# Optimization experiments

Measured on AMD Instinct MI355X. Metric: run time of the kernel, lower is better.

The kernel has to match this reference:

```python
import jax, jax.numpy as jnp
import numpy as np

E, B, T = 7, 50, 100               # ensemble (network_size), no_batches=50, time blocks
D, A, L, H, C = 128, 32, 256, 1024, 128  # data, action, latent, hidden, context sizes
H_STEP = 0.1                        # (t1 - t0) / T == dt -> one SDE step per block


def setup_inputs() -> dict:
    key = jax.random.key(0)
    ks = iter(jax.random.split(key, 64))
    def nrm(shape, scale=1.0):
        return jax.random.normal(next(ks), shape, jnp.float32) * scale
    def ens(i, o):
        s = 1.0 / np.sqrt(i)
        return nrm((E, i, o), s), nrm((E, o), s)
    def lin(i, o):
        s = 1.0 / np.sqrt(i)
        return nrm((i, o), s), nrm((o,), s)
    inp = {}
    inp["enc_w1"], inp["enc_b1"] = ens(D, H)
    inp["enc_w2"], inp["enc_b2"] = ens(H, H)
    inp["enc_w3"], inp["enc_b3"] = ens(H, C)
    inp["qz0_w"], inp["qz0_b"] = ens(C, 2 * L)
    inp["act_w"], inp["act_b"] = ens(L + A + D, L)
    inp["proj_w1"], inp["proj_b1"] = ens(L, H)
    inp["proj_w2"], inp["proj_b2"] = ens(H, H)
    inp["proj_w3"], inp["proj_b3"] = ens(H, D)
    inp["f_w1"], inp["f_b1"] = lin(L, H)
    inp["f_w2"], inp["f_b2"] = lin(H, H)
    inp["f_w3"], inp["f_b3"] = lin(H, L)
    inp["h_w1"], inp["h_b1"] = lin(L, H)
    inp["h_w2"], inp["h_b2"] = lin(H, H)
    inp["h_w3"], inp["h_b3"] = lin(H, L)
    # per-latent-dim g nets: Linear(1,H) -> ReLU -> Linear(H,1), stacked over L dims
    inp["g_w1"] = nrm((L, H), 0.2)
    inp["g_b1"] = nrm((L, H), 0.2)
    inp["g_w2"] = nrm((L, H), 0.2 / np.sqrt(H))
    inp["g_b2"] = 0.5 + nrm((L,), 0.01)   # keep diffusion bounded away from 0
    inp["pz0_mean"] = jnp.zeros((E, 1, L), jnp.float32)
    inp["pz0_logstd"] = jnp.zeros((E, 1, L), jnp.float32)
    inp["xs"] = nrm((E, T * B, D))
    inp["actions"] = nrm((E, T * B, A))
    inp["eps_z0"] = nrm((T, E, B, L))      # torch.randn_like noise for z0 reparam
    inp["dw_noise"] = nrm((T, E * B, L))   # Brownian increment noise (unit std)
    return inp


def reference(enc_w1, enc_b1, enc_w2, enc_b2, enc_w3, enc_b3,
              qz0_w, qz0_b, act_w, act_b,
              proj_w1, proj_b1, proj_w2, proj_b2, proj_w3, proj_b3,
              f_w1, f_b1, f_w2, f_b2, f_w3, f_b3,
              h_w1, h_b1, h_w2, h_b2, h_w3, h_b3,
              g_w1, g_b1, g_w2, g_b2,
              pz0_mean, pz0_logstd,
              xs, actions, eps_z0, dw_noise):
    def ens_lin(x, w, b):  # EnsembleFC: bmm + bias
        return jnp.einsum('ebi,eio->ebo', x, w) + b[:, None, :]

    def encoder(x):
        x = jax.nn.relu(ens_lin(x, enc_w1, enc_b1))
        x = jax.nn.relu(ens_lin(x, enc_w2, enc_b2))
        return ens_lin(x, enc_w3, enc_b3)

    def projector(z):
        z = jnp.tanh(ens_lin(z, proj_w1, proj_b1))
        z = jnp.tanh(ens_lin(z, proj_w2, proj_b2))
        return ens_lin(z, proj_w3, proj_b3)

    def mlp(y, w1, b1, w2, b2, w3, b3):  # Linear-ReLU-Linear-Tanh-Linear
        y = jax.nn.relu(y @ w1 + b1)
        y = jnp.tanh(y @ w2 + b2)
        return y @ w3 + b3

    def g_fn(y):  # vectorized per-dim tiny MLPs: y (N, L) -> (N, L)
        hh = jax.nn.relu(y[:, :, None] * g_w1[None] + g_b1[None])  # (N, L, H)
        return jnp.sum(hh * g_w2[None], axis=-1) + g_b2

    xs_t = jnp.moveaxis(xs.reshape(E, T, B, D), 1, 0)        # (T, E, B, D)
    act_t = jnp.moveaxis(actions.reshape(E, T, B, A), 1, 0)  # (T, E, B, A)
    sqrt_h = jnp.sqrt(jnp.float32(H_STEP))

    def step(carry, inps):
        zs_last, i = carry
        x_i, a_i, eps_i, dw_i = inps
        ctx = encoder(x_i)                                  # (E, B, C)
        q = ens_lin(ctx, qz0_w, qz0_b)                      # (E, B, 2L)
        qm, ql = q[..., :L], q[..., L:]
        z0 = qm + jnp.exp(ql) * eps_i
        z_in = jnp.where(i == 0, z0, zs_last)               # first step uses z0
        lad = jnp.concatenate([z_in, a_i, x_i], axis=2)
        z = ens_lin(lad, act_w, act_b).reshape(E * B, L)
        # one SDE step with logqp (f: posterior drift, h: prior drift, g: diffusion)
        fv = mlp(z, f_w1, f_b1, f_w2, f_b2, f_w3, f_b3)
        hv = mlp(z, h_w1, h_b1, h_w2, h_b2, h_w3, h_b3)
        gv = g_fn(z)
        u = (fv - hv) / gv
        lr = 0.5 * jnp.sum(u * u, axis=-1) * H_STEP         # (E*B,) log-ratio increment
        z_new = z + fv * H_STEP + gv * (sqrt_h * dw_i)
        zs_new = z_new.reshape(E, B, L)
        xm = projector(zs_new)                              # (E, B, D)
        # KL(q(z0) || p(z0)) for diagonal Gaussians
        kl = (pz0_logstd - ql) \
             + (jnp.exp(2.0 * ql) + (qm - pz0_mean) ** 2) / (2.0 * jnp.exp(2.0 * pz0_logstd)) \
             - 0.5
        logqp0 = kl.sum(axis=2).mean(axis=1)                # (E,)
        lr_mean = lr.reshape(E, B).mean(axis=1)             # (E,)
        return (zs_new, i + 1), (lr_mean, logqp0, xm)

    init = (jnp.zeros((E, B, L), xs.dtype), jnp.int32(0))
    (_, _), (lrm, lq0, xms) = jax.lax.scan(step, init, (xs_t, act_t, eps_z0, dw_noise))
    logqp_path = lrm.sum(axis=0) + lq0.sum(axis=0)          # (E,)
    predicted_xs = jnp.moveaxis(xms, 0, 1).reshape(E, T * B, D)
    return logqp_path, predicted_xs
```

## Files before the change

kernel.cpp:

```cpp
#include <hip/hip_runtime.h>
#include <hip/hip_bf16.h>
#include <math.h>

#define E_ 7
#define B_ 50
#define T_ 100
#define D_ 128
#define A_ 32
#define L_ 256
#define H_ 1024
#define C_ 128
#define EB_ 350
#define TB_ 5000
#define SQRTH 0.31622776601683794f

typedef __attribute__((ext_vector_type(8))) short s8v;
typedef __attribute__((ext_vector_type(4))) float f32x4;
typedef _Float16 f16x2 __attribute__((ext_vector_type(2)));
typedef __hip_bfloat16 bf16;

#define MFMA __builtin_amdgcn_mfma_f32_16x16x32_bf16

__device__ __forceinline__ int lswz(int row, int ck) {
  return (((ck & ~7) | ((ck ^ row) & 7)) << 3);
}
__device__ __forceinline__ int swzE(int r, int col) {
  const int ck = col >> 3;
  return (((ck & ~7) | ((ck ^ r) & 7)) << 3) + (col & 7);
}

struct BG {
  const bf16* A[8];
  const bf16* W[8];
  const float* bias[8];
  float* Cf[8];
  bf16* Cb[8];
};

template<int BM, int ACT, int OUT>
__global__ __launch_bounds__(256)
void bgemm(BG g, int M, int K, int lda, int ldw, int ldc) {
  __shared__ short As[BM * 64];
  __shared__ short Ws[128 * 64];
  const short* Ap = (const short*)g.A[blockIdx.z];
  const short* Wp = (const short*)g.W[blockIdx.z];
  const int bm = blockIdx.x * BM, bn = blockIdx.y * 128;
  const int tid = threadIdx.x;
  const int wv = tid >> 6, lane = tid & 63;
  const int wm0 = (wv >> 1) * (BM / 2), wn0 = (wv & 1) * 64;
  const int l15 = lane & 15, l4 = lane >> 4;
  constexpr int FM = BM / 32;
// ... 50 lines not shown
  float* Cf = g.Cf[blockIdx.z];
  bf16* Cb = g.Cb[blockIdx.z];
#pragma unroll
  for (int n = 0; n < 4; ++n) {
    const int col = bn + wn0 + n * 16 + l15;
    const float bv = bias ? bias[col] : 0.f;
#pragma unroll
    for (int m = 0; m < FM; ++m) {
#pragma unroll
      for (int j = 0; j < 4; ++j) {
        const int row = bm + wm0 + m * 16 + l4 * 4 + j;
        if (row < M) {
          float v = acc[m][n][j] + bv;
          if (ACT == 1) v = fmaxf(v, 0.f);
          if (ACT == 2) v = tanhf(v);
          if (OUT == 0) Cf[(size_t)row * ldc + col] = v;
          if (OUT == 1) Cb[(size_t)row * ldc + col] = __float2bfloat16(v);
        }
      }
    }
  }
}

__global__ __launch_bounds__(256)
void cvtT_kernel(const float* __restrict__ src, bf16* __restrict__ dst,
                 int K, int N, long ss, long ds) {
  __shared__ float t[32][33];
  src += (size_t)blockIdx.z * ss;
  dst += (size_t)blockIdx.z * ds;
  const int n0 = blockIdx.x * 32, k0 = blockIdx.y * 32;
  const int tx = threadIdx.x & 31, ty = threadIdx.x >> 5;
#pragma unroll
  for (int i = 0; i < 4; ++i)
    t[ty + 8 * i][tx] = src[(size_t)(k0 + ty + 8 * i) * N + n0 + tx];
  __syncthreads();
#pragma unroll
  for (int i = 0; i < 4; ++i)
    dst[(size_t)(n0 + ty + 8 * i) * K + k0 + tx] = __float2bfloat16(t[tx][ty + 8 * i]);
}

struct B4 { bf16 a, b, c, d; };
__global__ __launch_bounds__(256)
void cvt_kernel(const float* __restrict__ s, bf16* __restrict__ d, int n4) {
  const int i = blockIdx.x * 256 + threadIdx.x;
  if (i < n4) {
    const float4 v = ((const float4*)s)[i];
    B4 o = {__float2bfloat16(v.x), __float2bfloat16(v.y),
            __float2bfloat16(v.z), __float2bfloat16(v.w)};
    ((B4*)d)[i] = o;
  }
}

__global__ __launch_bounds__(256)
void packW(const float* __restrict__ src, bf16* __restrict__ dst, int K, int N) {
  const int idx = blockIdx.x * 256 + threadIdx.x;
  if (idx >= K * N) return;
  const int k = idx / N, n = idx - k * N;
  const size_t fo = ((size_t)(n >> 4) * (K >> 5) + (k >> 5)) * 512 +
                    (((k >> 3) & 3) << 7) + ((n & 15) << 3) + (k & 7);
  dst[fo] = __float2bfloat16(src[idx]);
}

__global__ __launch_bounds__(256)
void packWz(const float* __restrict__ act_w, bf16* __restrict__ hi, bf16* __restrict__ lo) {
  const int idx = blockIdx.x * 256 + threadIdx.x;
  if (idx >= E_ * 65536) return;
  const int e = idx >> 16, rem = idx & 65535, k = rem >> 8, n = rem & 255;
  const float w = act_w[(size_t)e * 416 * 256 + (size_t)k * 256 + n];
  const bf16 h = __float2bfloat16(w);
  const size_t fo = (size_t)e * 65536 + ((size_t)(n >> 4) * 8 + (k >> 5)) * 512 +
                    (((k >> 3) & 3) << 7) + ((n & 15) << 3) + (k & 7);
  hi[fo] = h;
  lo[fo] = __float2bfloat16(w - __bfloat162float(h));
}

__global__ __launch_bounds__(256)
void ax_build(const float* __restrict__ actions, const float* __restrict__ xs,
              bf16* __restrict__ dst) {
  const int idx = blockIdx.x * 256 + threadIdx.x;
  if (idx >= E_ * TB_ * 192) return;
  const int k = idx % 192;
  const int r = (idx / 192) % TB_;
  const int e = idx / (192 * TB_);
// ... 4 lines not shown
}

__global__ __launch_bounds__(256)
void waxT_build(const float* __restrict__ act_w, bf16* __restrict__ dst) {
  const int idx = blockIdx.x * 256 + threadIdx.x;
  if (idx >= E_ * 256 * 192) return;
  const int k = idx % 192;
  const int n = (idx / 192) % 256;
  const int e = idx / (192 * 256);
  float v = (k < 160) ? act_w[(size_t)e * 416 * 256 + (size_t)(256 + k) * 256 + n] : 0.f;
  dst[idx] = __float2bfloat16(v);
}

__global__ __launch_bounds__(256)
void gpack_build(const float* __restrict__ gw1, const float* __restrict__ gb1,
                 const float* __restrict__ gw2, _Float16* __restrict__ dst) {
  const int idx = blockIdx.x * 256 + threadIdx.x;
  if (idx >= 256 * 3 * 1024) return;
  const int l = idx / 3072, rem = idx - l * 3072, arr = rem >> 10, h = rem & 1023;
  const float* s = arr == 0 ? gw1 : (arr == 1 ? gb1 : gw2);
  dst[idx] = (_Float16)s[(size_t)l * 1024 + h];
}

__global__ __launch_bounds__(256)
void qkl_kernel(const float* __restrict__ ctx, int rows, int row_off, int ctx_estride,
                const float* __restrict__ qw, const float* __restrict__ qb,
                const float* __restrict__ pm, const float* __restrict__ pl,
                const float* __restrict__ eps0, bf16* __restrict__ z0hi,
                bf16* __restrict__ z0lo, float* __restrict__ logqp) {
  __shared__ float cx[16][128];
  __shared__ float red[16];
  const int e = blockIdx.y;
  const int r0 = blockIdx.x * 16;
  const int tid = threadIdx.x;
  {
    const int r = tid >> 4, c = (tid & 15) * 8;
    float4 v0 = make_float4(0.f, 0.f, 0.f, 0.f), v1 = v0;
    if (r0 + r < rows) {
      const float* src = ctx + (size_t)e * ctx_estride + (size_t)(r0 + r) * C_ + c;
      v0 = *(const float4*)src;
      v1 = *(const float4*)(src + 4);
    }
    *(float4*)&cx[r][c] = v0;
    *(float4*)&cx[r][c + 4] = v1;
  }
  if (tid < 16) red[tid] = 0.f;
  __syncthreads();
  const int j = tid;
  const float* w = qw + (size_t)e * C_ * 512;
  float am_[16] = {};
  float al_[16] = {};
  for (int k0 = 0; k0 < C_; k0 += 4) {
    float wm[4], wl[4];
#pragma unroll
    for (int q = 0; q < 4; ++q) {
      wm[q] = w[(size_t)(k0 + q) * 512 + j];
      wl[q] = w[(size_t)(k0 + q) * 512 + 256 + j];
// ... 18 lines not shown
  for (int r = 0; r < 16; ++r) {
    float kl = 0.f;
    if (r0 + r < rows) {
      const float qm_ = am_[r] + qbm;
      const float ql_ = al_[r] + qbl;
      const float dm = qm_ - pmv;
      kl = plv - ql_ + (expf(2.f * ql_) + dm * dm) * inv2e - 0.5f;
      const int gi = row_off + r0 + r;
      if (gi < B_) {
        const size_t zi = ((size_t)e * B_ + gi) * L_ + j;
        const float z0 = qm_ + expf(ql_) * eps0[zi];
        const bf16 h = __float2bfloat16(z0);
        z0hi[zi] = h;
        z0lo[zi] = __float2bfloat16(z0 - __bfloat162float(h));
      }
    }
    for (int off = 32; off; off >>= 1) kl += __shfl_xor(kl, off, 64);
    if ((tid & 63) == 0) atomicAdd(&red[r], kl);
  }
  __syncthreads();
  if (tid < 16 && r0 + tid < rows) atomicAdd(&logqp[e], red[tid] * (1.0f / B_));
}

__global__ __launch_bounds__(256, 2)
void k1_act(const bf16* __restrict__ zhi, const bf16* __restrict__ zlo,
            const bf16* __restrict__ wzh, const bf16* __restrict__ wzl,
            const float* __restrict__ axw, float* __restrict__ zP,
            bf16* __restrict__ zPb, int t) {
  __shared__ short Ah[16 * 256];
  __shared__ short Al[16 * 256];
  const int e = blockIdx.z, rb = blockIdx.x, nb = blockIdx.y * 128;
  const int r0 = rb * 13;
  const int nrows = (50 - r0 < 13) ? (50 - r0) : 13;
  const int tid = threadIdx.x, lane = tid & 63, wv = tid >> 6;
  const int l15 = lane & 15, l4 = lane >> 4;
  const short* zh = (const short*)zhi + (size_t)(e * 50 + r0) * 256;
  const short* zl = (const short*)zlo + (size_t)(e * 50 + r0) * 256;
#pragma unroll
  for (int i = 0; i < 2; ++i) {
    const int lin = tid + i * 256, row = lin >> 5, ck = lin & 31;
    s8v vh = {}, vl = {};
    if (row < nrows) {
      vh = *(const s8v*)(zh + row * 256 + ck * 8);
      vl = *(const s8v*)(zl + row * 256 + ck * 8);
    }
    *(s8v*)(Ah + row * 256 + lswz(row, ck)) = vh;
    *(s8v*)(Al + row * 256 + lswz(row, ck)) = vl;
  }
  __syncthreads();
  const short* Bh = (const short*)wzh + (size_t)e * 65536;
  const short* Bl = (const short*)wzl + (size_t)e * 65536;
  f32x4 acc[2] = {};
#pragma unroll
  for (int kt = 0; kt < 8; ++kt) {
    const int ck = kt * 4 + l4;
    const s8v ah = *(const s8v*)(Ah + l15 * 256 + lswz(l15, ck));
    const s8v al = *(const s8v*)(Al + l15 * 256 + lswz(l15, ck));
// ... 7 lines not shown
      acc[nt] = MFMA(al, bh, acc[nt], 0, 0, 0);
      acc[nt] = MFMA(ah, bl, acc[nt], 0, 0, 0);
    }
  }
#pragma unroll
  for (int nt = 0; nt < 2; ++nt) {
    const int col = nb + wv * 32 + nt * 16 + l15;
#pragma unroll
    for (int j = 0; j < 4; ++j) {
      const int row = l4 * 4 + j;
      if (row < nrows) {
        const int gr = e * 50 + r0 + row;
        const float v = acc[nt][j] + axw[((size_t)e * TB_ + t * 50 + r0 + row) * 256 + col];
        zP[(size_t)gr * 256 + col] = v;
        zPb[(size_t)gr * 256 + col] = __float2bfloat16(v);
      }
    }
  }
}

__global__ __launch_bounds__(256, 2)
void k2_l1(const bf16* __restrict__ zPb, const bf16* __restrict__ w1f,
           const float* __restrict__ fb1, const float* __restrict__ hb1,
           bf16* __restrict__ fh1) {
  __shared__ short As[16 * 256];
  const int rb = blockIdx.x, nb = blockIdx.y * 128;
  const int r0 = rb * 16;
  const int tid = threadIdx.x, lane = tid & 63, wv = tid >> 6;
  const int l15 = lane & 15, l4 = lane >> 4;
#pragma unroll
  for (int i = 0; i < 2; ++i) {
    const int lin = tid + i * 256, row = lin >> 5, ck = lin & 31;
    s8v v = {};
    if (r0 + row < EB_)
      v = *(const s8v*)((const short*)zPb + (size_t)(r0 + row) * 256 + ck * 8);
    *(s8v*)(As + row * 256 + lswz(row, ck)) = v;
  }
  __syncthreads();
  f32x4 acc[2] = {};
#pragma unroll
  for (int kt = 0; kt < 8; ++kt) {
    const int ck = kt * 4 + l4;
    const s8v a = *(const s8v*)(As + l15 * 256 + lswz(l15, ck));
#pragma unroll
    for (int nt = 0; nt < 2; ++nt) {
      const int ng = nb + wv * 32 + nt * 16;
      const s8v b = *(const s8v*)((const short*)w1f + ((size_t)(ng >> 4) * 8 + kt) * 512 + lane * 8);
      acc[nt] = MFMA(a, b, acc[nt], 0, 0, 0);
    }
  }
#pragma unroll
  for (int nt = 0; nt < 2; ++nt) {
    const int col = nb + wv * 32 + nt * 16 + l15;
    const float bv = (col < 1024) ? fb1[col] : hb1[col - 1024];
#pragma unroll
    for (int j = 0; j < 4; ++j) {
      const int row = r0 + l4 * 4 + j;
      if (row < EB_)
        fh1[(size_t)row * 2048 + col] = __float2bfloat16(fmaxf(acc[nt][j] + bv, 0.f));
    }
  }
}

__global__ __launch_bounds__(256, 2)
void k3g(const bf16* __restrict__ fh1, const bf16* __restrict__ w2f,
         const float* __restrict__ fb2, const float* __restrict__ hb2,
         bf16* __restrict__ fh2, const float* __restrict__ zP,
         const _Float16* __restrict__ gpk, const float* __restrict__ gb2,
         float* __restrict__ gv) {
  __shared__ short As[16 * 1024];
  const int rb = blockIdx.x, nbl = blockIdx.y;
  const int tid = threadIdx.x, lane = tid & 63, wv = tid >> 6;
  const int l15 = lane & 15, l4 = lane >> 4;
  const int r0 = rb * 16;
  if (nbl >= 16) {
    float* ztile = (float*)As;
    const int c0 = (nbl - 16) * 64;
#pragma unroll
    for (int i = 0; i < 4; ++i) {
      const int lin = tid + i * 256, row = lin >> 6, col = lin & 63;
      ztile[row * 64 + col] =
          (r0 + row < EB_) ? zP[(size_t)(r0 + row) * 256 + c0 + col] : 1.0f;
    }
    __syncthreads();
    const int lloc = tid >> 2, hq = tid & 3;
    const _Float16* gl = gpk + (size_t)(c0 + lloc) * 3072 + hq * 256;
    f16x2 z2[16];
#pragma unroll
    for (int r = 0; r < 16; ++r) {
      const _Float16 zh_ = (_Float16)ztile[r * 64 + lloc];
      z2[r] = f16x2{zh_, zh_};
    }
    float ga[16] = {};
    for (int hp = 0; hp < 128; ++hp) {
      const f16x2 w1v = *(const f16x2*)(gl + 2 * hp);
      const f16x2 b1v = *(const f16x2*)(gl + 1024 + 2 * hp);
      const f16x2 w2v = *(const f16x2*)(gl + 2048 + 2 * hp);
// ... 46 lines not shown
      const s8v b = *(const s8v*)((const short*)w2f + ((size_t)(ng >> 4) * 32 + kt) * 512 + lane * 8);
      acc[nt] = MFMA(a, b, acc[nt], 0, 0, 0);
    }
  }
#pragma unroll
  for (int nt = 0; nt < 2; ++nt) {
    const int col = nb + wv * 32 + nt * 16 + l15;
    const float bv = half ? hb2[col - 1024] : fb2[col];
#pragma unroll
    for (int j = 0; j < 4; ++j) {
      const int row = r0 + l4 * 4 + j;
      if (row < EB_)
        fh2[(size_t)row * 2048 + col] = __float2bfloat16(tanhf(acc[nt][j] + bv));
    }
  }
}

__global__ __launch_bounds__(256, 1)
void k4_fin(const bf16* __restrict__ fh2, const bf16* __restrict__ w3f,
            const float* __restrict__ fb3, const float* __restrict__ hb3,
            const float* __restrict__ gv, const float* __restrict__ zP,
            const float* __restrict__ dw, bf16* __restrict__ zhi,
            bf16* __restrict__ zlo, bf16* __restrict__ zs_bf,
            float* __restrict__ logqp, int t) {
  __shared__ short As[16 * 1024];
  __shared__ float ztile[16][64];
  __shared__ float ebuck[8];
  const int rb = blockIdx.x, cb = blockIdx.y;
  const int r0 = rb * 16, c0 = cb * 64;
  const int tid = threadIdx.x, lane = tid & 63, wv = tid >> 6;
  const int l15 = lane & 15, l4 = lane >> 4;
  if (tid < 8) ebuck[tid] = 0.f;
#pragma unroll
  for (int i = 0; i < 4; ++i) {
    const int lin = tid + i * 256, row = lin >> 6, col = lin & 63;
    ztile[row][col] = (r0 + row < EB_) ? zP[(size_t)(r0 + row) * 256 + c0 + col] : 1.0f;
  }
  f32x4 accF = {}, accH = {};
#pragma unroll
  for (int fb = 0; fb < 2; ++fb) {
    __syncthreads();
#pragma unroll
    for (int i = 0; i < 8; ++i) {
      const int lin = tid + i * 256, row = lin >> 7, ck = lin & 127;
      s8v v = {};
      if (r0 + row < EB_)
        v = *(const s8v*)((const short*)fh2 + (size_t)(r0 + row) * 2048 + fb * 1024 + ck * 8);
      *(s8v*)(As + row * 1024 + lswz(row, ck)) = v;
    }
    __syncthreads();
    const int ng = fb * 256 + c0 + wv * 16;
    f32x4 acc = {};
#pragma unroll 4
    for (int kt = 0; kt < 32; ++kt) {
// ... 20 lines not shown
                         gvv * (SQRTH * dw[(size_t)t * (EB_ * 256) + (size_t)row * 256 + col]);
      const bf16 h = __float2bfloat16(znew);
      const size_t zi = (size_t)row * 256 + col;
      zhi[zi] = h;
      zlo[zi] = __float2bfloat16(znew - __bfloat162float(h));
      const int e = row / 50, b = row - e * 50;
      zs_bf[((size_t)e * TB_ + t * 50 + b) * 256 + col] = h;
    }
  }
  __syncthreads();
  if (tid < 7) {
    const float v = ebuck[tid];
    if (v != 0.f) atomicAdd(&logqp[tid], v);
  }
}

__global__ void init_kernel(float* logqp) {
  if (threadIdx.x < E_) logqp[threadIdx.x] = 0.f;
}

extern "C" void kernel_launch(void* const* d_in, const int* in_sizes, int n_in,
                              void* d_out, int out_size, void* d_ws, size_t ws_size,
                              hipStream_t stream) {
  (void)in_sizes; (void)n_in; (void)out_size;
  const float* enc_w1 = (const float*)d_in[0];
  const float* enc_b1 = (const float*)d_in[1];
  const float* enc_w2 = (const float*)d_in[2];
  const float* enc_b2 = (const float*)d_in[3];
  const float* enc_w3 = (const float*)d_in[4];
  const float* enc_b3 = (const float*)d_in[5];
  const float* qz0_w  = (const float*)d_in[6];
  const float* qz0_b  = (const float*)d_in[7];
  const float* act_w  = (const float*)d_in[8];
  const float* act_b  = (const float*)d_in[9];
  const float* proj_w1 = (const float*)d_in[10];
  const float* proj_b1 = (const float*)d_in[11];
  const float* proj_w2 = (const float*)d_in[12];
  const float* proj_b2 = (const float*)d_in[13];
  const float* proj_w3 = (const float*)d_in[14];
  const float* proj_b3 = (const float*)d_in[15];
  const float* f_w1 = (const float*)d_in[16];
  const float* f_b1 = (const float*)d_in[17];
  const float* f_w2 = (const float*)d_in[18];
  const float* f_b2 = (const float*)d_in[19];
  const float* f_w3 = (const float*)d_in[20];
  const float* f_b3 = (const float*)d_in[21];
  const float* h_w1 = (const float*)d_in[22];
// ... 22 lines not shown
  auto alloc = [&](size_t bytes) {
    void* p = base + off;
    off = (off + bytes + 255) & ~(size_t)255;
    return p;
  };
  bf16* zhi    = (bf16*)alloc((size_t)EB_ * 256 * 2);
  bf16* zlo    = (bf16*)alloc((size_t)EB_ * 256 * 2);
  float* zP    = (float*)alloc((size_t)EB_ * 256 * 4);
  bf16* zPb    = (bf16*)alloc((size_t)EB_ * 256 * 2);
  bf16* fh1    = (bf16*)alloc((size_t)EB_ * 2048 * 2);
  bf16* fh2    = (bf16*)alloc((size_t)EB_ * 2048 * 2);
  float* gvb   = (float*)alloc((size_t)EB_ * 256 * 4);
  bf16* zs_bf  = (bf16*)alloc((size_t)E_ * T_ * B_ * 256 * 2);
  float* axw   = (float*)alloc((size_t)E_ * TB_ * 256 * 4);
  bf16* ax_bf  = (bf16*)alloc((size_t)E_ * TB_ * 192 * 2);
  bf16* waxT   = (bf16*)alloc((size_t)E_ * 256 * 192 * 2);
  bf16* wzh    = (bf16*)alloc((size_t)E_ * 65536 * 2);
  bf16* wzl    = (bf16*)alloc((size_t)E_ * 65536 * 2);
  bf16* w1f    = (bf16*)alloc((size_t)2048 * 256 * 2);
  bf16* w2f    = (bf16*)alloc((size_t)2048 * 1024 * 2);
  bf16* w3f    = (bf16*)alloc((size_t)512 * 1024 * 2);
  _Float16* gpk = (_Float16*)alloc((size_t)256 * 3 * 1024 * 2);
  bf16* xs_bf  = (bf16*)alloc((size_t)E_ * TB_ * D_ * 2);
  bf16* ew1T = (bf16*)alloc((size_t)E_ * D_ * H_ * 2);
  bf16* ew2T = (bf16*)alloc((size_t)E_ * H_ * H_ * 2);
  bf16* ew3T = (bf16*)alloc((size_t)E_ * H_ * C_ * 2);
  bf16* pw1T = (bf16*)alloc((size_t)E_ * L_ * H_ * 2);
  bf16* pw2T = (bf16*)alloc((size_t)E_ * H_ * H_ * 2);
  bf16* pw3T = (bf16*)alloc((size_t)E_ * H_ * D_ * 2);
  const size_t per_row = (size_t)E_ * (H_ * 2 * 2 + C_ * 4);
  size_t remain = (ws_size > off + 4096) ? (ws_size - off - 4096) : 0;
  int CH = (int)(remain / per_row);
  if (CH > 2500) CH = 2500;
  if (CH < 64) CH = 64;
  bf16* bufA = (bf16*)alloc((size_t)E_ * CH * H_ * 2);
  bf16* bufB = (bf16*)alloc((size_t)E_ * CH * H_ * 2);
  float* bufC = (float*)alloc((size_t)E_ * CH * C_ * 4);

  init_kernel<<<dim3(1), dim3(64), 0, stream>>>(logqp);

  const dim3 cb256(256);
  cvt_kernel<<<dim3((E_ * TB_ * D_ / 4 + 255) / 256), cb256, 0, stream>>>(xs, xs_bf, E_ * TB_ * D_ / 4);
  cvtT_kernel<<<dim3(H_ / 32, D_ / 32, E_), cb256, 0, stream>>>(enc_w1, ew1T, D_, H_, (long)D_ * H_, (long)D_ * H_);
  cvtT_kernel<<<dim3(H_ / 32, H_ / 32, E_), cb256, 0, stream>>>(enc_w2, ew2T, H_, H_, (long)H_ * H_, (long)H_ * H_);
  cvtT_kernel<<<dim3(C_ / 32, H_ / 32, E_), cb256, 0, stream>>>(enc_w3, ew3T, H_, C_, (long)H_ * C_, (long)H_ * C_);
  cvtT_kernel<<<dim3(H_ / 32, L_ / 32, E_), cb256, 0, stream>>>(proj_w1, pw1T, L_, H_, (long)L_ * H_, (long)L_ * H_);
  cvtT_kernel<<<dim3(H_ / 32, H_ / 32, E_), cb256, 0, stream>>>(proj_w2, pw2T, H_, H_, (long)H_ * H_, (long)H_ * H_);
  cvtT_kernel<<<dim3(D_ / 32, H_ / 32, E_), cb256, 0, stream>>>(proj_w3, pw3T, H_, D_, (long)H_ * D_, (long)H_ * D_);
  ax_build<<<dim3((E_ * TB_ * 192 + 255) / 256), cb256, 0, stream>>>(actions, xs, ax_bf);
  waxT_build<<<dim3((E_ * 256 * 192 + 255) / 256), cb256, 0, stream>>>(act_w, waxT);
  packWz<<<dim3((E_ * 65536 + 255) / 256), cb256, 0, stream>>>(act_w, wzh, wzl);
  packW<<<dim3((256 * 1024 + 255) / 256), cb256, 0, stream>>>(f_w1, w1f, 256, 1024);
  packW<<<dim3((256 * 1024 + 255) / 256), cb256, 0, stream>>>(h_w1, w1f + (size_t)1024 * 256, 256, 1024);
  packW<<<dim3((1024 * 1024 + 255) / 256), cb256, 0, stream>>>(f_w2, w2f, 1024, 1024);
  packW<<<dim3((1024 * 1024 + 255) / 256), cb256, 0, stream>>>(h_w2, w2f + (size_t)1024 * 1024, 1024, 1024);
  packW<<<dim3((1024 * 256 + 255) / 256), cb256, 0, stream>>>(f_w3, w3f, 1024, 256);
  packW<<<dim3((1024 * 256 + 255) / 256), cb256, 0, stream>>>(h_w3, w3f + (size_t)256 * 1024, 1024, 256);
  gpack_build<<<dim3((256 * 3 * 1024 + 255) / 256), cb256, 0, stream>>>(g_w1, g_b1, g_w2, gpk);

  BG g;
  for (int e = 0; e < E_; ++e) {
    g.A[e] = ax_bf + (size_t)e * TB_ * 192;
    g.W[e] = waxT + (size_t)e * 256 * 192;
    g.bias[e] = act_b + (size_t)e * 256;
    g.Cf[e] = axw + (size_t)e * TB_ * 256;
  }
  bgemm<128, 0, 0><<<dim3((TB_ + 127) / 128, 2, E_), 256, 0, stream>>>(g, TB_, 192, 192, 192, 256);

  for (int c = 0; c < TB_; c += CH) {
    const int rows = (TB_ - c < CH) ? (TB_ - c) : CH;
    const int mt = (rows + 127) / 128;
    for (int e = 0; e < E_; ++e) {
      g.A[e] = xs_bf + ((size_t)e * TB_ + c) * D_;
      g.W[e] = ew1T + (size_t)e * D_ * H_;
      g.bias[e] = enc_b1 + (size_t)e * H_;
      g.Cb[e] = bufA + (size_t)e * CH * H_;
    }
    bgemm<128, 1, 1><<<dim3(mt, H_ / 128, E_), 256, 0, stream>>>(g, rows, D_, D_, D_, H_);
    for (int e = 0; e < E_; ++e) {
      g.A[e] = bufA + (size_t)e * CH * H_;
      g.W[e] = ew2T + (size_t)e * H_ * H_;
      g.bias[e] = enc_b2 + (size_t)e * H_;
      g.Cb[e] = bufB + (size_t)e * CH * H_;
    }
    bgemm<128, 1, 1><<<dim3(mt, H_ / 128, E_), 256, 0, stream>>>(g, rows, H_, H_, H_, H_);
    for (int e = 0; e < E_; ++e) {
      g.A[e] = bufB + (size_t)e * CH * H_;
      g.W[e] = ew3T + (size_t)e * H_ * C_;
      g.bias[e] = enc_b3 + (size_t)e * C_;
      g.Cf[e] = bufC + (size_t)e * CH * C_;
    }
    bgemm<128, 0, 0><<<dim3(mt, C_ / 128, E_), 256, 0, stream>>>(g, rows, H_, H_, H_, C_);
    qkl_kernel<<<dim3((rows + 15) / 16, E_), 256, 0, stream>>>(
        bufC, rows, c, CH * C_, qz0_w, qz0_b, pz0_mean, pz0_logstd, eps_z0,
        zhi, zlo, logqp);
  }

  for (int t = 0; t < T_; ++t) {
    k1_act<<<dim3(4, 2, E_), 256, 0, stream>>>(zhi, zlo, wzh, wzl, axw, zP, zPb, t);
    k2_l1<<<dim3(22, 16), 256, 0, stream>>>(zPb, w1f, f_b1, h_b1, fh1);
    k3g<<<dim3(22, 20), 256, 0, stream>>>(fh1, w2f, f_b2, h_b2, fh2,
                                          zP, gpk, g_b2, gvb);
    k4_fin<<<dim3(22, 4), 256, 0, stream>>>(fh2, w3f, f_b3, h_b3, gvb,
                                            zP, dw, zhi, zlo, zs_bf, logqp, t);
  }

  for (int c = 0; c < TB_; c += CH) {
    const int rows = (TB_ - c < CH) ? (TB_ - c) : CH;
    const int mt = (rows + 127) / 128;
    for (int e = 0; e < E_; ++e) {
      g.A[e] = zs_bf + ((size_t)e * T_ * B_ + c) * L_;
      g.W[e] = pw1T + (size_t)e * L_ * H_;
      g.bias[e] = proj_b1 + (size_t)e * H_;
      g.Cb[e] = bufA + (size_t)e * CH * H_;
    }
    bgemm<128, 2, 1><<<dim3(mt, H_ / 128, E_), 256, 0, stream>>>(g, rows, L_, L_, L_, H_);
    for (int e = 0; e < E_; ++e) {
      g.A[e] = bufA + (size_t)e * CH * H_;
      g.W[e] = pw2T + (size_t)e * H_ * H_;
      g.bias[e] = proj_b2 + (size_t)e * H_;
      g.Cb[e] = bufB + (size_t)e * CH * H_;
    }
    bgemm<128, 2, 1><<<dim3(mt, H_ / 128, E_), 256, 0, stream>>>(g, rows, H_, H_, H_, H_);
    for (int e = 0; e < E_; ++e) {
      g.A[e] = bufB + (size_t)e * CH * H_;
      g.W[e] = pw3T + (size_t)e * H_ * D_;
      g.bias[e] = proj_b3 + (size_t)e * D_;
      g.Cf[e] = pred + ((size_t)e * TB_ + c) * D_;
    }
    bgemm<128, 0, 0><<<dim3(mt, D_ / 128, E_), 256, 0, stream>>>(g, rows, H_, H_, H_, D_);
  }
}
```

Measured before the change: 9.915 ms.

## Overlap encoder and projector GEMMs with the sequential SDE step kernels

Removes the separate batched encoder and projector GEMM phases. Each of the four per-step SDE kernels now carries extra blocks that process an encoder chunk (layer1/layer2/layer3/qkl staged across t mod 4) or a software-pipelined projector stage for earlier time steps. The idea is to fill idle CUs during the latency-bound recurrent loop so the throughput-bound GEMMs come almost for free. In exchange it uses small 16-row MFMA tiles with direct global weight loads, which are much less efficient than the big tiled GEMMs. It also adds more blocks that may contend with the critical-path kernels.

Measured after the change: 11.27 ms. 13.7% more time.

```diff
diff --git a/kernel.cpp b/kernel.cpp
--- a/kernel.cpp
+++ b/kernel.cpp
@@ -13,6 +13,7 @@
 #define EB_ 350
 #define TB_ 5000
 #define SQRTH 0.31622776601683794f
+#define MC 198
 
 typedef __attribute__((ext_vector_type(8))) short s8v;
 typedef __attribute__((ext_vector_type(4))) float f32x4;
@@ -23,10 +24,6 @@
 
 __device__ __forceinline__ int lswz(int row, int ck) {
   return (((ck & ~7) | ((ck ^ row) & 7)) << 3);
-}
-__device__ __forceinline__ int swzE(int r, int col) {
-  const int ck = col >> 3;
-  return (((ck & ~7) | ((ck ^ r) & 7)) << 3) + (col & 7);
 }
 
 struct BG {
@@ -123,21 +120,63 @@
   }
 }
 
-__global__ __launch_bounds__(256)
-void cvtT_kernel(const float* __restrict__ src, bf16* __restrict__ dst,
-                 int K, int N, long ss, long ds) {
-  __shared__ float t[32][33];
-  src += (size_t)blockIdx.z * ss;
-  dst += (size_t)blockIdx.z * ds;
-  const int n0 = blockIdx.x * 32, k0 = blockIdx.y * 32;
-  const int tx = threadIdx.x & 31, ty = threadIdx.x >> 5;
-#pragma unroll
-  for (int i = 0; i < 4; ++i)
-    t[ty + 8 * i][tx] = src[(size_t)(k0 + ty + 8 * i) * N + n0 + tx];
+__device__ void tile_gemm(short* As, const short* Arow, int nrows, int lda, int K,
+                          const short* Wf, int ngBase, const float* bias,
+                          float* CfRow0, bf16* CbRow0, int ldc, int act, int tid) {
+  const int lane = tid & 63, wv = tid >> 6, l15 = lane & 15, l4 = lane >> 4;
+  const int K8 = K >> 3;
+  for (int i = tid; i < (K8 << 4); i += 256) {
+    const int row = i / K8, ck = i - row * K8;
+    s8v v = {};
+    if (row < nrows) v = *(const s8v*)(Arow + (size_t)row * lda + ck * 8);
+    *(s8v*)(As + row * K + lswz(row, ck)) = v;
+  }
   __syncthreads();
-#pragma unroll
-  for (int i = 0; i < 4; ++i)
-    dst[(size_t)(n0 + ty + 8 * i) * K + k0 + tx] = __float2bfloat16(t[tx][ty + 8 * i]);
+  const int Kt = K >> 5;
+  f32x4 acc0 = {}, acc1 = {};
+  const int ng0 = ngBase + wv * 2;
+  for (int kt = 0; kt < Kt; ++kt) {
+    const int ck = kt * 4 + l4;
+    const s8v a = *(const s8v*)(As + l15 * K + lswz(l15, ck));
+    const s8v b0 = *(const s8v*)(Wf + ((size_t)(ng0 * Kt + kt)) * 512 + (size_t)lane * 8);
+    const s8v b1 = *(const s8v*)(Wf + ((size_t)((ng0 + 1) * Kt + kt)) * 512 + (size_t)lane * 8);
+    acc0 = MFMA(a, b0, acc0, 0, 0, 0);
+    acc1 = MFMA(a, b1, acc1, 0, 0, 0);
+  }
+#pragma unroll
+  for (int nt = 0; nt < 2; ++nt) {
+    const f32x4 acc = nt ? acc1 : acc0;
+    const int col = (ng0 + nt) * 16 + l15;
+    const float bv = bias ? bias[col] : 0.f;
+#pragma unroll
+    for (int j = 0; j < 4; ++j) {
+      const int r = l4 * 4 + j;
+      if (r < nrows) {
+        float v = acc[j] + bv;
+        if (act == 1) v = fmaxf(v, 0.f);
+        if (act == 2) v = tanhf(v);
+        if (CbRow0) CbRow0[(size_t)r * ldc + col] = __float2bfloat16(v);
+        else CfRow0[(size_t)r * ldc + col] = v;
+      }
+    }
+  }
+}
+
+__global__ __launch_bounds__(256)
+void sgemm_e(const bf16* Abf, long aEstride, long aBase, int lda, int nrowsPerE,
+             const bf16* Wf, long wEstride, int K,
+             const float* bias, int bEstride,
+             float* Cf, bf16* Cb, long cEstride, long cBase, int ldc, int act) {
+  __shared__ short As[16 * 1024];
+  const int rt = blockIdx.x, ntb = blockIdx.y, e = blockIdx.z;
+  const int r0 = rt * 16;
+  int nrows = nrowsPerE - r0;
+  if (nrows > 16) nrows = 16;
+  const size_t co = (size_t)e * cEstride + cBase + (size_t)r0 * ldc;
+  tile_gemm(As, (const short*)Abf + (size_t)e * aEstride + aBase + (size_t)r0 * lda,
+            nrows, lda, K, (const short*)Wf + (size_t)e * wEstride, ntb * 8,
+            bias + (size_t)e * bEstride,
+            Cf ? Cf + co : nullptr, Cb ? Cb + co : nullptr, ldc, act, threadIdx.x);
 }
 
 struct B4 { bf16 a, b, c, d; };
@@ -160,6 +199,18 @@
   const size_t fo = ((size_t)(n >> 4) * (K >> 5) + (k >> 5)) * 512 +
                     (((k >> 3) & 3) << 7) + ((n & 15) << 3) + (k & 7);
   dst[fo] = __float2bfloat16(src[idx]);
+}
+
+__global__ __launch_bounds__(256)
+void packWE(const float* __restrict__ src, bf16* __restrict__ dst, int K, int N,
+            long sE, long dE) {
+  const int e = blockIdx.z;
+  const int idx = blockIdx.x * 256 + threadIdx.x;
+  if (idx >= K * N) return;
+  const int k = idx / N, n = idx - k * N;
+  const size_t fo = ((size_t)(n >> 4) * (K >> 5) + (k >> 5)) * 512 +
+                    (((k >> 3) & 3) << 7) + ((n & 15) << 3) + (k & 7);
+  dst[(size_t)e * dE + fo] = __float2bfloat16(src[(size_t)e * sE + idx]);
 }
 
 __global__ __launch_bounds__(256)
@@ -210,17 +261,13 @@
   dst[idx] = (_Float16)s[(size_t)l * 1024 + h];
 }
 
-__global__ __launch_bounds__(256)
-void qkl_kernel(const float* __restrict__ ctx, int rows, int row_off, int ctx_estride,
-                const float* __restrict__ qw, const float* __restrict__ qb,
-                const float* __restrict__ pm, const float* __restrict__ pl,
-                const float* __restrict__ eps0, bf16* __restrict__ z0hi,
-                bf16* __restrict__ z0lo, float* __restrict__ logqp) {
-  __shared__ float cx[16][128];
-  __shared__ float red[16];
-  const int e = blockIdx.y;
-  const int r0 = blockIdx.x * 16;
-  const int tid = threadIdx.x;
+__device__ void qkl_dev(char* Ubuf, int e, int r0,
+                        const float* ctx, int rows, int row_off, int ctx_estride,
+                        const float* qw, const float* qb, const float* pm,
+                        const float* pl, const float* eps0,
+                        bf16* z0hi, bf16* z0lo, float* logqp, int tid) {
+  float (*cx)[128] = (float(*)[128])Ubuf;
+  float* red = (float*)(Ubuf + 16 * 128 * 4);
   {
     const int r = tid >> 4, c = (tid & 15) * 8;
     float4 v0 = make_float4(0.f, 0.f, 0.f, 0.f), v1 = v0;
@@ -285,17 +332,42 @@
   if (tid < 16 && r0 + tid < rows) atomicAdd(&logqp[e], red[tid] * (1.0f / B_));
 }
 
+__global__ __launch_bounds__(256)
+void qkl_kernel(const float* ctx, int rows, int row_off, int ctx_estride,
+                const float* qw, const float* qb, const float* pm, const float* pl,
+                const float* eps0, bf16* z0hi, bf16* z0lo, float* logqp) {
+  __shared__ char U[16 * 128 * 4 + 64];
+  qkl_dev(U, blockIdx.y, blockIdx.x * 16, ctx, rows, row_off, ctx_estride,
+          qw, qb, pm, pl, eps0, z0hi, z0lo, logqp, threadIdx.x);
+}
+
 __global__ __launch_bounds__(256, 2)
 void k1_act(const bf16* __restrict__ zhi, const bf16* __restrict__ zlo,
             const bf16* __restrict__ wzh, const bf16* __restrict__ wzl,
             const float* __restrict__ axw, float* __restrict__ zP,
-            bf16* __restrict__ zPb, int t) {
-  __shared__ short Ah[16 * 256];
-  __shared__ short Al[16 * 256];
+            bf16* __restrict__ zPb,
+            const bf16* __restrict__ pbuf2, const bf16* __restrict__ pw3f,
+            const float* __restrict__ proj_b3, float* __restrict__ pred, int t) {
+  __shared__ short U[16 * 1024];
+  const int tid = threadIdx.x;
+  if (blockIdx.y == 2) {
+    if (t < 2) return;
+    const int tp = t - 2, rt = blockIdx.x, e = blockIdx.z;
+    int nrows = 50 - rt * 16;
+    if (nrows > 16) nrows = 16;
+    tile_gemm(U, (const short*)pbuf2 + (size_t)(e * 50 + rt * 16) * 1024,
+              nrows, 1024, 1024, (const short*)pw3f + (size_t)e * 131072, 0,
+              proj_b3 + (size_t)e * 128,
+              pred + (size_t)e * 640000 + (size_t)(tp * 50 + rt * 16) * 128,
+              nullptr, 128, 0, tid);
+    return;
+  }
+  short* Ah = U;
+  short* Al = U + 4096;
   const int e = blockIdx.z, rb = blockIdx.x, nb = blockIdx.y * 128;
   const int r0 = rb * 13;
   const int nrows = (50 - r0 < 13) ? (50 - r0) : 13;
-  const int tid = threadIdx.x, lane = tid & 63, wv = tid >> 6;
+  const int lane = tid & 63, wv = tid >> 6;
   const int l15 = lane & 15, l4 = lane >> 4;
   const short* zh = (const short*)zhi + (size_t)(e * 50 + r0) * 256;
   const short* zl = (const short*)zlo + (size_t)(e * 50 + r0) * 256;
@@ -349,11 +421,64 @@
 __global__ __launch_bounds__(256, 2)
 void k2_l1(const bf16* __restrict__ zPb, const bf16* __restrict__ w1f,
            const float* __restrict__ fb1, const float* __restrict__ hb1,
-           bf16* __restrict__ fh1) {
-  __shared__ short As[16 * 256];
-  const int rb = blockIdx.x, nb = blockIdx.y * 128;
+           bf16* __restrict__ fh1,
+           const bf16* __restrict__ xs_bf,
+           const bf16* __restrict__ ew1f, const float* __restrict__ enc_b1,
+           bf16* __restrict__ ebuf1,
+           const bf16* __restrict__ ew2f, const float* __restrict__ enc_b2,
+           bf16* __restrict__ ebuf2,
+           const bf16* __restrict__ ew3f, const float* __restrict__ enc_b3,
+           float* __restrict__ ctxb,
+           const float* __restrict__ qw, const float* __restrict__ qb,
+           const float* __restrict__ pm, const float* __restrict__ pl,
+           const float* __restrict__ eps0, bf16* __restrict__ zhi,
+           bf16* __restrict__ zlo, float* __restrict__ logqp, int t) {
+  __shared__ short U[16 * 1024];
+  const int tid = threadIdx.x;
+  const int x = blockIdx.x, y = blockIdx.y;
+  if (y >= 16) {
+    const int sid = (y - 16) * 22 + x;
+    const int mode = t & 3, chunk = t >> 2;
+    if (chunk >= 25) return;
+    const int rowBase = 50 + chunk * MC;
+    if (mode <= 1) {
+      if (sid >= 728) return;
+      const int e = sid / 104, rem = sid - e * 104, rt = rem >> 3, ntb = rem & 7;
+      int nrows = MC - rt * 16;
+      if (nrows > 16) nrows = 16;
+      if (mode == 0) {
+        tile_gemm(U, (const short*)xs_bf + (size_t)e * (TB_ * 128) +
+                      (size_t)(rowBase + rt * 16) * 128,
+                  nrows, 128, 128, (const short*)ew1f + (size_t)e * 131072, ntb * 8,
+                  enc_b1 + (size_t)e * 1024, nullptr,
+                  ebuf1 + (size_t)(e * MC + rt * 16) * 1024, 1024, 1, tid);
+      } else {
+        tile_gemm(U, (const short*)ebuf1 + (size_t)(e * MC + rt * 16) * 1024,
+                  nrows, 1024, 1024, (const short*)ew2f + (size_t)e * 1048576, ntb * 8,
+                  enc_b2 + (size_t)e * 1024, nullptr,
+                  ebuf2 + (size_t)(e * MC + rt * 16) * 1024, 1024, 1, tid);
+      }
+    } else if (mode == 2) {
+      if (sid >= 91) return;
+      const int e = sid / 13, rt = sid - e * 13;
+      int nrows = MC - rt * 16;
+      if (nrows > 16) nrows = 16;
+      tile_gemm(U, (const short*)ebuf2 + (size_t)(e * MC + rt * 16) * 1024,
+                nrows, 1024, 1024, (const short*)ew3f + (size_t)e * 131072, 0,
+                enc_b3 + (size_t)e * 128,
+                ctxb + (size_t)(e * MC + rt * 16) * 128, nullptr, 128, 0, tid);
+    } else {
+      if (sid >= 91) return;
+      const int e = sid / 13, rt = sid - e * 13;
+      qkl_dev((char*)U, e, rt * 16, ctxb, MC, rowBase, MC * 128,
+              qw, qb, pm, pl, eps0, zhi, zlo, logqp, tid);
+    }
+    return;
+  }
+  short* As = U;
+  const int rb = x, nb = y * 128;
   const int r0 = rb * 16;
-  const int tid = threadIdx.x, lane = tid & 63, wv = tid >> 6;
+  const int lane = tid & 63, wv = tid >> 6;
   const int l15 = lane & 15, l4 = lane >> 4;
 #pragma unroll
   for (int i = 0; i < 2; ++i) {
@@ -394,12 +519,28 @@
          const float* __restrict__ fb2, const float* __restrict__ hb2,
          bf16* __restrict__ fh2, const float* __restrict__ zP,
          const _Float16* __restrict__ gpk, const float* __restrict__ gb2,
-         float* __restrict__ gv) {
+         float* __restrict__ gv,
+         const bf16* __restrict__ zs_bf, const bf16* __restrict__ pw1f,
+         const float* __restrict__ proj_b1, bf16* __restrict__ pbuf1, int t) {
   __shared__ short As[16 * 1024];
   const int rb = blockIdx.x, nbl = blockIdx.y;
   const int tid = threadIdx.x, lane = tid & 63, wv = tid >> 6;
   const int l15 = lane & 15, l4 = lane >> 4;
   const int r0 = rb * 16;
+  if (nbl >= 20) {
+    if (t < 1) return;
+    const int sid = (nbl - 20) * 22 + rb;
+    if (sid >= 224) return;
+    const int e = sid / 32, rem = sid - e * 32, rt = rem >> 3, ntb = rem & 7;
+    int nrows = 50 - rt * 16;
+    if (nrows > 16) nrows = 16;
+    tile_gemm(As, (const short*)zs_bf + (size_t)e * (TB_ * 256) +
+                  (size_t)((t - 1) * 50 + rt * 16) * 256,
+              nrows, 256, 256, (const short*)pw1f + (size_t)e * 262144, ntb * 8,
+              proj_b1 + (size_t)e * 1024, nullptr,
+              pbuf1 + (size_t)(e * 50 + rt * 16) * 1024, 1024, 2, tid);
+    return;
+  }
   if (nbl >= 16) {
     float* ztile = (float*)As;
     const int c0 = (nbl - 16) * 64;
@@ -492,14 +633,29 @@
             const float* __restrict__ gv, const float* __restrict__ zP,
             const float* __restrict__ dw, bf16* __restrict__ zhi,
             bf16* __restrict__ zlo, bf16* __restrict__ zs_bf,
-            float* __restrict__ logqp, int t) {
+            float* __restrict__ logqp,
+            const bf16* __restrict__ pbuf1, const bf16* __restrict__ pw2f,
+            const float* __restrict__ proj_b2, bf16* __restrict__ pbuf2, int t) {
   __shared__ short As[16 * 1024];
   __shared__ float ztile[16][64];
   __shared__ float ebuck[8];
+  const int tid = threadIdx.x, lane = tid & 63, wv = tid >> 6;
+  const int l15 = lane & 15, l4 = lane >> 4;
+  if (blockIdx.y >= 4) {
+    if (t < 1) return;
+    const int sid = (blockIdx.y - 4) * 22 + blockIdx.x;
+    if (sid >= 224) return;
+    const int e = sid / 32, rem = sid - e * 32, rt = rem >> 3, ntb = rem & 7;
+    int nrows = 50 - rt * 16;
+    if (nrows > 16) nrows = 16;
+    tile_gemm(As, (const short*)pbuf1 + (size_t)(e * 50 + rt * 16) * 1024,
+              nrows, 1024, 1024, (const short*)pw2f + (size_t)e * 1048576, ntb * 8,
+              proj_b2 + (size_t)e * 1024, nullptr,
+              pbuf2 + (size_t)(e * 50 + rt * 16) * 1024, 1024, 2, tid);
+    return;
+  }
   const int rb = blockIdx.x, cb = blockIdx.y;
   const int r0 = rb * 16, c0 = cb * 64;
-  const int tid = threadIdx.x, lane = tid & 63, wv = tid >> 6;
-  const int l15 = lane & 15, l4 = lane >> 4;
   if (tid < 8) ebuck[tid] = 0.f;
 #pragma unroll
   for (int i = 0; i < 4; ++i) {
@@ -566,7 +722,7 @@
 extern "C" void kernel_launch(void* const* d_in, const int* in_sizes, int n_in,
                               void* d_out, int out_size, void* d_ws, size_t ws_size,
                               hipStream_t stream) {
-  (void)in_sizes; (void)n_in; (void)out_size;
+  (void)in_sizes; (void)n_in; (void)out_size; (void)ws_size;
   const float* enc_w1 = (const float*)d_in[0];
   const float* enc_b1 = (const float*)d_in[1];
   const float* enc_w2 = (const float*)d_in[2];
@@ -635,31 +791,25 @@
   bf16* w3f    = (bf16*)alloc((size_t)512 * 1024 * 2);
   _Float16* gpk = (_Float16*)alloc((size_t)256 * 3 * 1024 * 2);
   bf16* xs_bf  = (bf16*)alloc((size_t)E_ * TB_ * D_ * 2);
-  bf16* ew1T = (bf16*)alloc((size_t)E_ * D_ * H_ * 2);
-  bf16* ew2T = (bf16*)alloc((size_t)E_ * H_ * H_ * 2);
-  bf16* ew3T = (bf16*)alloc((size_t)E_ * H_ * C_ * 2);
-  bf16* pw1T = (bf16*)alloc((size_t)E_ * L_ * H_ * 2);
-  bf16* pw2T = (bf16*)alloc((size_t)E_ * H_ * H_ * 2);
-  bf16* pw3T = (bf16*)alloc((size_t)E_ * H_ * D_ * 2);
-  const size_t per_row = (size_t)E_ * (H_ * 2 * 2 + C_ * 4);
-  size_t remain = (ws_size > off + 4096) ? (ws_size - off - 4096) : 0;
-  int CH = (int)(remain / per_row);
-  if (CH > 2500) CH = 2500;
-  if (CH < 64) CH = 64;
-  bf16* bufA = (bf16*)alloc((size_t)E_ * CH * H_ * 2);
-  bf16* bufB = (bf16*)alloc((size_t)E_ * CH * H_ * 2);
-  float* bufC = (float*)alloc((size_t)E_ * CH * C_ * 4);
+  bf16* ew1f = (bf16*)alloc((size_t)E_ * 131072 * 2);
+  bf16* ew2f = (bf16*)alloc((size_t)E_ * 1048576 * 2);
+  bf16* ew3f = (bf16*)alloc((size_t)E_ * 131072 * 2);
+  bf16* pw1f = (bf16*)alloc((size_t)E_ * 262144 * 2);
+  bf16* pw2f = (bf16*)alloc((size_t)E_ * 1048576 * 2);
+  bf16* pw3f = (bf16*)alloc((size_t)E_ * 131072 * 2);
+  bf16* ebuf1 = (bf16*)alloc((size_t)E_ * MC * 1024 * 2);
+  bf16* ebuf2 = (bf16*)alloc((size_t)E_ * MC * 1024 * 2);
+  float* ctxb = (float*)alloc((size_t)E_ * MC * 128 * 4);
+  bf16* bb1   = (bf16*)alloc((size_t)E_ * 50 * 1024 * 2);
+  bf16* bb2   = (bf16*)alloc((size_t)E_ * 50 * 1024 * 2);
+  float* ctx0 = (float*)alloc((size_t)E_ * 50 * 128 * 4);
+  bf16* pbuf1 = (bf16*)alloc((size_t)350 * 1024 * 2);
+  bf16* pbuf2 = (bf16*)alloc((size_t)350 * 1024 * 2);
 
   init_kernel<<<dim3(1), dim3(64), 0, stream>>>(logqp);
 
   const dim3 cb256(256);
   cvt_kernel<<<dim3((E_ * TB_ * D_ / 4 + 255) / 256), cb256, 0, stream>>>(xs, xs_bf, E_ * TB_ * D_ / 4);
-  cvtT_kernel<<<dim3(H_ / 32, D_ / 32, E_), cb256, 0, stream>>>(enc_w1, ew1T, D_, H_, (long)D_ * H_, (long)D_ * H_);
-  cvtT_kernel<<<dim3(H_ / 32, H_ / 32, E_), cb256, 0, stream>>>(enc_w2, ew2T, H_, H_, (long)H_ * H_, (long)H_ * H_);
-  cvtT_kernel<<<dim3(C_ / 32, H_ / 32, E_), cb256, 0, stream>>>(enc_w3, ew3T, H_, C_, (long)H_ * C_, (long)H_ * C_);
-  cvtT_kernel<<<dim3(H_ / 32, L_ / 32, E_), cb256, 0, stream>>>(proj_w1, pw1T, L_, H_, (long)L_ * H_, (long)L_ * H_);
-  cvtT_kernel<<<dim3(H_ / 32, H_ / 32, E_), cb256, 0, stream>>>(proj_w2, pw2T, H_, H_, (long)H_ * H_, (long)H_ * H_);
-  cvtT_kernel<<<dim3(D_ / 32, H_ / 32, E_), cb256, 0, stream>>>(proj_w3, pw3T, H_, D_, (long)H_ * D_, (long)H_ * D_);
   ax_build<<<dim3((E_ * TB_ * 192 + 255) / 256), cb256, 0, stream>>>(actions, xs, ax_bf);
   waxT_build<<<dim3((E_ * 256 * 192 + 255) / 256), cb256, 0, stream>>>(act_w, waxT);
   packWz<<<dim3((E_ * 65536 + 255) / 256), cb256, 0, stream>>>(act_w, wzh, wzl);
@@ -670,6 +820,12 @@
   packW<<<dim3((1024 * 256 + 255) / 256), cb256, 0, stream>>>(f_w3, w3f, 1024, 256);
   packW<<<dim3((1024 * 256 + 255) / 256), cb256, 0, stream>>>(h_w3, w3f + (size_t)256 * 1024, 1024, 256);
   gpack_build<<<dim3((256 * 3 * 1024 + 255) / 256), cb256, 0, stream>>>(g_w1, g_b1, g_w2, gpk);
+  packWE<<<dim3(512, 1, E_), cb256, 0, stream>>>(enc_w1, ew1f, 128, 1024, 131072, 131072);
+  packWE<<<dim3(4096, 1, E_), cb256, 0, stream>>>(enc_w2, ew2f, 1024, 1024, 1048576, 1048576);
+  packWE<<<dim3(512, 1, E_), cb256, 0, stream>>>(enc_w3, ew3f, 1024, 128, 131072, 131072);
+  packWE<<<dim3(1024, 1, E_), cb256, 0, stream>>>(proj_w1, pw1f, 256, 1024, 262144, 262144);
+  packWE<<<dim3(4096, 1, E_), cb256, 0, stream>>>(proj_w2, pw2f, 1024, 1024, 1048576, 1048576);
+  packWE<<<dim3(512, 1, E_), cb256, 0, stream>>>(proj_w3, pw3f, 1024, 128, 131072, 131072);
 
   BG g;
   for (int e = 0; e < E_; ++e) {
@@ -680,67 +836,46 @@
   }
   bgemm<128, 0, 0><<<dim3((TB_ + 127) / 128, 2, E_), 256, 0, stream>>>(g, TB_, 192, 192, 192, 256);
 
-  for (int c = 0; c < TB_; c += CH) {
-    const int rows = (TB_ - c < CH) ? (TB_ - c) : CH;
-    const int mt = (rows + 127) / 128;
-    for (int e = 0; e < E_; ++e) {
-      g.A[e] = xs_bf + ((size_t)e * TB_ + c) * D_;
-      g.W[e] = ew1T + (size_t)e * D_ * H_;
-      g.bias[e] = enc_b1 + (size_t)e * H_;
-      g.Cb[e] = bufA + (size_t)e * CH * H_;
-    }
-    bgemm<128, 1, 1><<<dim3(mt, H_ / 128, E_), 256, 0, stream>>>(g, rows, D_, D_, D_, H_);
-    for (int e = 0; e < E_; ++e) {
-      g.A[e] = bufA + (size_t)e * CH * H_;
-      g.W[e] = ew2T + (size_t)e * H_ * H_;
-      g.bias[e] = enc_b2 + (size_t)e * H_;
-      g.Cb[e] = bufB + (size_t)e * CH * H_;
-    }
-    bgemm<128, 1, 1><<<dim3(mt, H_ / 128, E_), 256, 0, stream>>>(g, rows, H_, H_, H_, H_);
-    for (int e = 0; e < E_; ++e) {
-      g.A[e] = bufB + (size_t)e * CH * H_;
-      g.W[e] = ew3T + (size_t)e * H_ * C_;
-      g.bias[e] = enc_b3 + (size_t)e * C_;
-      g.Cf[e] = bufC + (size_t)e * CH * C_;
-    }
-    bgemm<128, 0, 0><<<dim3(mt, C_ / 128, E_), 256, 0, stream>>>(g, rows, H_, H_, H_, C_);
-    qkl_kernel<<<dim3((rows + 15) / 16, E_), 256, 0, stream>>>(
-        bufC, rows, c, CH * C_, qz0_w, qz0_b, pz0_mean, pz0_logstd, eps_z0,
-        zhi, zlo, logqp);
-  }
+  sgemm_e<<<dim3(4, 8, E_), cb256, 0, stream>>>(
+      xs_bf, (long)TB_ * 128, 0, 128, 50, ew1f, 131072, 128, enc_b1, 1024,
+      nullptr, bb1, 51200, 0, 1024, 1);
+  sgemm_e<<<dim3(4, 8, E_), cb256, 0, stream>>>(
+      bb1, 51200, 0, 1024, 50, ew2f, 1048576, 1024, enc_b2, 1024,
+      nullptr, bb2, 51200, 0, 1024, 1);
+  sgemm_e<<<dim3(4, 1, E_), cb256, 0, stream>>>(
+      bb2, 51200, 0, 1024, 50, ew3f, 131072, 1024, enc_b3, 128,
+      ctx0, nullptr, 6400, 0, 128, 0);
+  qkl_kernel<<<dim3(4, E_), cb256, 0, stream>>>(
+      ctx0, 50, 0, 6400, qz0_w, qz0_b, pz0_mean, pz0_logstd, eps_z0,
+      zhi, zlo, logqp);
 
   for (int t = 0; t < T_; ++t) {
-    k1_act<<<dim3(4, 2, E_), 256, 0, stream>>>(zhi, zlo, wzh, wzl, axw, zP, zPb, t);
-    k2_l1<<<dim3(22, 16), 256, 0, stream>>>(zPb, w1f, f_b1, h_b1, fh1);
-    k3g<<<dim3(22, 20), 256, 0, stream>>>(fh1, w2f, f_b2, h_b2, fh2,
-                                          zP, gpk, g_b2, gvb);
-    k4_fin<<<dim3(22, 4), 256, 0, stream>>>(fh2, w3f, f_b3, h_b3, gvb,
-                                            zP, dw, zhi, zlo, zs_bf, logqp, t);
-  }
-
-  for (int c = 0; c < TB_; c += CH) {
-    const int rows = (TB_ - c < CH) ? (TB_ - c) : CH;
-    const int mt = (rows + 127) / 128;
-    for (int e = 0; e < E_; ++e) {
-      g.A[e] = zs_bf + ((size_t)e * T_ * B_ + c) * L_;
-      g.W[e] = pw1T + (size_t)e * L_ * H_;
-      g.bias[e] = proj_b1 + (size_t)e * H_;
-      g.Cb[e] = bufA + (size_t)e * CH * H_;
-    }
-    bgemm<128, 2, 1><<<dim3(mt, H_ / 128, E_), 256, 0, stream>>>(g, rows, L_, L_, L_, H_);
-    for (int e = 0; e < E_; ++e) {
-      g.A[e] = bufA + (size_t)e * CH * H_;
-      g.W[e] = pw2T + (size_t)e * H_ * H_;
-      g.bias[e] = proj_b2 + (size_t)e * H_;
-      g.Cb[e] = bufB + (size_t)e * CH * H_;
-    }
-    bgemm<128, 2, 1><<<dim3(mt, H_ / 128, E_), 256, 0, stream>>>(g, rows, H_, H_, H_, H_);
-    for (int e = 0; e < E_; ++e) {
-      g.A[e] = bufB + (size_t)e * CH * H_;
-      g.W[e] = pw3T + (size_t)e * H_ * D_;
-      g.bias[e] = proj_b3 + (size_t)e * D_;
-      g.Cf[e] = pred + ((size_t)e * TB_ + c) * D_;
-    }
-    bgemm<128, 0, 0><<<dim3(mt, D_ / 128, E_), 256, 0, stream>>>(g, rows, H_, H_, H_, D_);
-  }
-}
+    k1_act<<<dim3(4, 3, E_), cb256, 0, stream>>>(zhi, zlo, wzh, wzl, axw, zP, zPb,
+                                                 pbuf2, pw3f, proj_b3, pred, t);
+    k2_l1<<<dim3(22, 50), cb256, 0, stream>>>(zPb, w1f, f_b1, h_b1, fh1,
+                                              xs_bf, ew1f, enc_b1, ebuf1,
+                                              ew2f, enc_b2, ebuf2,
+                                              ew3f, enc_b3, ctxb,
+                                              qz0_w, qz0_b, pz0_mean, pz0_logstd,
+                                              eps_z0, zhi, zlo, logqp, t);
+    k3g<<<dim3(22, 31), cb256, 0, stream>>>(fh1, w2f, f_b2, h_b2, fh2,
+                                            zP, gpk, g_b2, gvb,
+                                            zs_bf, pw1f, proj_b1, pbuf1, t);
+    k4_fin<<<dim3(22, 15), cb256, 0, stream>>>(fh2, w3f, f_b3, h_b3, gvb,
+                                               zP, dw, zhi, zlo, zs_bf, logqp,
+                                               pbuf1, pw2f, proj_b2, pbuf2, t);
+  }
+
+  sgemm_e<<<dim3(4, 1, E_), cb256, 0, stream>>>(
+      pbuf2, 51200, 0, 1024, 50, pw3f, 131072, 1024, proj_b3, 128,
+      pred, nullptr, 640000, (long)98 * 50 * 128, 128, 0);
+  sgemm_e<<<dim3(4, 8, E_), cb256, 0, stream>>>(
+      zs_bf, (long)TB_ * 256, (long)99 * 50 * 256, 256, 50, pw1f, 262144, 256,
+      proj_b1, 1024, nullptr, pbuf1, 51200, 0, 1024, 2);
+  sgemm_e<<<dim3(4, 8, E_), cb256, 0, stream>>>(
+      pbuf1, 51200, 0, 1024, 50, pw2f, 1048576, 1024, proj_b2, 1024,
+      nullptr, pbuf2, 51200, 0, 1024, 2);
+  sgemm_e<<<dim3(4, 1, E_), cb256, 0, stream>>>(
+      pbuf2, 51200, 0, 1024, 50, pw3f, 131072, 1024, proj_b3, 128,
+      pred, nullptr, 640000, (long)99 * 50 * 128, 128, 0);
+}
```
